# Kernel optimization log

Measured on AMD Instinct MI355X. Metric: run time of the kernel, lower is better.

## Reference

```python
import jax, jax.numpy as jnp
import numpy as np

N, E, D = 50000, 800000, 128
LN_EPS = 1e-5


def setup_inputs() -> dict:
    key = jax.random.key(0)
    ks = jax.random.split(key, 6)
    return {
        "x": jax.random.normal(ks[0], (N, D), dtype=jnp.float32),
        "edge_index": jax.random.randint(ks[1], (2, E), 0, N, dtype=jnp.int64),
        "edge_weight": jax.random.uniform(ks[2], (E,), dtype=jnp.float32),
        "lin_w": jax.random.normal(ks[3], (D, D), dtype=jnp.float32) * (1.0 / np.sqrt(D)),
        "lin_b": jax.random.normal(ks[4], (D,), dtype=jnp.float32) * 0.02,
        "ln_gamma": jnp.ones((D,), dtype=jnp.float32),
        "ln_beta": jnp.zeros((D,), dtype=jnp.float32),
    }


def reference(x, edge_index, edge_weight, lin_w, lin_b, ln_gamma, ln_beta):
    n = x.shape[0]
    src, dst = edge_index[0], edge_index[1]
    # degree (by dst), symmetric-ish normalization with +1 smoothing
    deg = jax.ops.segment_sum(jnp.ones(dst.shape, x.dtype), dst, num_segments=n)
    dis = jax.lax.rsqrt(deg + 1.0)  # (N,)
    # gather -> scale -> scatter-add
    scale = (edge_weight * dis[src])[:, None]          # (E,1)
    msg = x[src] * scale                               # (E,D)
    agg = jax.ops.segment_sum(msg, dst, num_segments=n)  # (N,D)
    agg = agg * dis[:, None] + x                       # residual
    # dense tail: Linear -> GELU (exact, matches torch F.gelu) -> LayerNorm
    h = jax.nn.gelu(agg @ lin_w.T + lin_b, approximate=False)
    mu = jnp.mean(h, axis=-1, keepdims=True)
    var = jnp.mean(jnp.square(h - mu), axis=-1, keepdims=True)
    return (h - mu) * jax.lax.rsqrt(var + LN_EPS) * ln_gamma + ln_beta
```

## Files before the change

### kernel.cpp

```cpp
#include <hip/hip_runtime.h>
#include <hip/hip_fp16.h>
#include <math.h>

#define D 128
#define CAP 48
#define LDS_STRIDE 136
#define CHUNKS 256
#define BLDS 4096

typedef __bf16  bf16x8 __attribute__((ext_vector_type(8)));
typedef float   f32x4  __attribute__((ext_vector_type(4)));

static __device__ __forceinline__ unsigned short f2bf(float f) {
    unsigned int u = __float_as_uint(f);
    u = (u + 0x7fffu + ((u >> 16) & 1u)) >> 16;
    return (unsigned short)u;
}
static __device__ __forceinline__ unsigned int pack2bf(float lo, float hi) {
    return (unsigned int)f2bf(lo) | ((unsigned int)f2bf(hi) << 16);
}
static __device__ __forceinline__ float bflo(unsigned int u) { return __uint_as_float(u << 16); }
static __device__ __forceinline__ float bfhi(unsigned int u) { return __uint_as_float(u & 0xffff0000u); }


__global__ __launch_bounds__(256) void k_hist(const int* __restrict__ dst,
                                              int* __restrict__ H,
                                              int e_count, int cs, int nbk) {
    __shared__ int hist[1024];
    int tid = threadIdx.x, c = blockIdx.x;
    for (int b = tid; b < nbk; b += 256) hist[b] = 0;
    __syncthreads();
    int lo = c * cs, hi = min(lo + cs, e_count);
    for (int i = lo + tid; i < hi; i += 256) atomicAdd(&hist[dst[i] >> 6], 1);
    __syncthreads();
    for (int b = tid; b < nbk; b += 256) H[b * CHUNKS + c] = hist[b];
}

__global__ __launch_bounds__(256) void k_bsum(const int* __restrict__ a,
                                              int* __restrict__ bsum, int n) {
    int g = blockIdx.x * 256 + threadIdx.x;
    int lane = threadIdx.x & 63, wave = threadIdx.x >> 6;
    int v = (g < n) ? a[g] : 0;
    #pragma unroll
    for (int off = 32; off > 0; off >>= 1) v += __shfl_down(v, off);
    __shared__ int ws[4];
    if (lane == 0) ws[wave] = v;
    __syncthreads();
    if (threadIdx.x == 0) bsum[blockIdx.x] = ws[0] + ws[1] + ws[2] + ws[3];
}

__global__ __launch_bounds__(1024) void k_scan_bsum2(int* __restrict__ bsum, int nb) {
    int tid = threadIdx.x, lane = tid & 63, wave = tid >> 6;
    int v = (tid < nb) ? bsum[tid] : 0;
    int incl = v;
    #pragma unroll
    for (int off = 1; off < 64; off <<= 1) {
        int t = __shfl_up(incl, off);
        if (lane >= off) incl += t;
    }
    __shared__ int ws[16];
    if (lane == 63) ws[wave] = incl;
    __syncthreads();
    if (tid == 0) {
        int run = 0;
        #pragma unroll
        for (int i = 0; i < 16; ++i) { int t = ws[i]; ws[i] = run; run += t; }
    }
    __syncthreads();
    if (tid < nb) bsum[tid] = incl - v + ws[wave];
}

__global__ __launch_bounds__(256) void k_applyH(int* __restrict__ H,
                                                const int* __restrict__ bsum_excl, int m) {
    int g = blockIdx.x * 256 + threadIdx.x;
    int tid = threadIdx.x, lane = tid & 63, wave = tid >> 6;
    int v = (g < m) ? H[g] : 0;
    int incl = v;
    #pragma unroll
    for (int off = 1; off < 64; off <<= 1) {
        int t = __shfl_up(incl, off);
        if (lane >= off) incl += t;
    }
    __shared__ int ws[4];
    if (lane == 63) ws[wave] = incl;
    __syncthreads();
    int add = bsum_excl[blockIdx.x];
    for (int i = 0; i < wave; ++i) add += ws[i];
    if (g < m) H[g] = incl - v + add;
}

__global__ __launch_bounds__(256) void k_scatter(const int* __restrict__ src,
                                                 const int* __restrict__ dst,
                                                 const float* __restrict__ ew,
                                                 const int* __restrict__ H,
                                                 unsigned int* __restrict__ rec,
                                                 int e_count, int cs, int nbk) {
    __shared__ int cur[1024];
    int tid = threadIdx.x, c = blockIdx.x;
    for (int b = tid; b < nbk; b += 256) cur[b] = H[b * CHUNKS + c];
    __syncthreads();
    int lo = c * cs, hi = min(lo + cs, e_count);
    for (int i = lo + tid; i < hi; i += 256) {
        int d = dst[i];
        int s = src[i];
        unsigned int q = (unsigned int)(ew[i] * 1023.0f + 0.5f);
        unsigned int r = (q << 22) | ((unsigned int)(d & 63) << 16) | (unsigned int)s;
        int pos = atomicAdd(&cur[d >> 6], 1);
        rec[pos] = r;
    }
}

__global__ __launch_bounds__(256) void k_bucket_sort(unsigned int* __restrict__ rec,
                                                     const int* __restrict__ H,
                                                     int* __restrict__ deg,
                                                     int* __restrict__ offs,
                                                     int e_count, int n, int nbk) {
    __shared__ int hist[64], curs[64];
    __shared__ unsigned int srt[BLDS];
    int tid = threadIdx.x, b = blockIdx.x;
    int start = H[b * CHUNKS];
    int end = (b == nbk - 1) ? e_count : H[(b + 1) * CHUNKS];
    int cnt = min(end - start, BLDS);
    if (tid < 64) hist[tid] = 0;
    __syncthreads();
    for (int i = tid; i < cnt; i += 256) atomicAdd(&hist[(rec[start + i] >> 16) & 63], 1);
    __syncthreads();
    if (tid < 64) {
        int dg = hist[tid];
        int incl = dg;
        #pragma unroll
        for (int off = 1; off < 64; off <<= 1) {
            int t = __shfl_up(incl, off);
            if (tid >= off) incl += t;
        }
        int excl = incl - dg;
        curs[tid] = excl;
        int node = b * 64 + tid;
        if (node < n) {
            deg[node] = dg;
            offs[node] = start + excl;
            if (node == n - 1) offs[n] = e_count;
        }
    }
    __syncthreads();
    for (int i = tid; i < cnt; i += 256) {
        unsigned int r = rec[start + i];
        int rank = atomicAdd(&curs[(r >> 16) & 63], 1);
        srt[rank] = r;
    }
    __syncthreads();
    for (int i = tid; i < cnt; i += 256) rec[start + i] = srt[i];
}


__global__ __launch_bounds__(256) void k_cast(const float* __restrict__ x,
                                              const int* __restrict__ deg,
                                              unsigned short* __restrict__ xs, int n) {
    int i4 = blockIdx.x * 256 + threadIdx.x;
    int nq = n * (D / 4);
    if (i4 >= nq) return;
    int node = i4 >> 5;
    float dd = rsqrtf((float)deg[node] + 1.0f);
    float4 v = ((const float4*)x)[i4];
    ushort4 u;
    u.x = f2bf(v.x * dd); u.y = f2bf(v.y * dd);
    u.z = f2bf(v.z * dd); u.w = f2bf(v.w * dd);
    ((ushort4*)xs)[i4] = u;
}


__global__ __launch_bounds__(256) void k_gather_csr(const unsigned short* __restrict__ xs,
                                                    const float* __restrict__ x,
                                                    const int* __restrict__ offs,
                                                    const unsigned int* __restrict__ rec,
                                                    unsigned short* __restrict__ aggbf, int n) {
    int node = (int)((blockIdx.x * blockDim.x + threadIdx.x) >> 6);
    int lane = threadIdx.x & 63;
    if (node >= n) return;
    int beg = offs[node], end = offs[node + 1];
    const float wq = 1.0f / 1023.0f;
    float ax = 0.f, ay = 0.f;

    int e = beg;
    for (; e + 3 < end; e += 4) {
        unsigned int r0 = rec[e + 0], r1 = rec[e + 1], r2 = rec[e + 2], r3 = rec[e + 3];
        unsigned int u0 = ((const unsigned int*)(xs + (size_t)(r0 & 0xffffu) * D))[lane];
        unsigned int u1 = ((const unsigned int*)(xs + (size_t)(r1 & 0xffffu) * D))[lane];
        unsigned int u2 = ((const unsigned int*)(xs + (size_t)(r2 & 0xffffu) * D))[lane];
        unsigned int u3 = ((const unsigned int*)(xs + (size_t)(r3 & 0xffffu) * D))[lane];
        float w0 = (float)(r0 >> 22) * wq;
        float w1 = (float)(r1 >> 22) * wq;
        float w2 = (float)(r2 >> 22) * wq;
        float w3 = (float)(r3 >> 22) * wq;
        ax += w0 * bflo(u0); ay += w0 * bfhi(u0);
        ax += w1 * bflo(u1); ay += w1 * bfhi(u1);
        ax += w2 * bflo(u2); ay += w2 * bfhi(u2);
        ax += w3 * bflo(u3); ay += w3 * bfhi(u3);
    }
    for (; e < end; ++e) {
        unsigned int r = rec[e];
        unsigned int u = ((const unsigned int*)(xs + (size_t)(r & 0xffffu) * D))[lane];
        float w = (float)(r >> 22) * wq;
        ax += w * bflo(u); ay += w * bfhi(u);
    }

    float dd = rsqrtf((float)(end - beg) + 1.0f);
    float2 xv = ((const float2*)(x + (size_t)node * D))[lane];
    ((unsigned int*)(aggbf + (size_t)node * D))[lane] = pack2bf(ax * dd + xv.x, ay * dd + xv.y);
}


__global__ __launch_bounds__(256) void k_tail_bf(const unsigned short* __restrict__ aggbf,
                                                 float* __restrict__ out,
                                                 const float* __restrict__ W,
                                                 const float* __restrict__ bias,
                                                 const float* __restrict__ gamma,
                                                 const float* __restrict__ beta, int n) {
    __shared__ unsigned short Bl[128 * LDS_STRIDE];

    int tid  = threadIdx.x;
    int lane = tid & 63;
    int wave = tid >> 6;
    int n16  = lane & 15;
    int quad = lane >> 4;

    #pragma unroll
    for (int it = 0; it < 16; ++it) {
        int idx4 = it * 256 + tid;
        float4 w4 = ((const float4*)W)[idx4];
        int t  = idx4 >> 5;
        int k4 = (idx4 & 31) << 2;
        ushort4 u;
        u.x = f2bf(w4.x); u.y = f2bf(w4.y); u.z = f2bf(w4.z); u.w = f2bf(w4.w);
        *(ushort4*)&Bl[t * LDS_STRIDE + k4] = u;
    }
    __syncthreads();

    int row0w = blockIdx.x * 64 + wave * 16;
    int arow  = row0w + n16;

    bf16x8 afr[4];
    #pragma unroll
    for (int ko = 0; ko < 4; ++ko)
        afr[ko] = __builtin_bit_cast(bf16x8,
            *(const uint4*)&aggbf[(size_t)arow * D + ko * 32 + quad * 8]);

    f32x4 acc[8];
    #pragma unroll
    for (int nt = 0; nt < 8; ++nt) acc[nt] = (f32x4){0.f, 0.f, 0.f, 0.f};

    #pragma unroll
    for (int nt = 0; nt < 8; ++nt) {
        #pragma unroll
        for (int ko = 0; ko < 4; ++ko) {
            bf16x8 bfr = __builtin_bit_cast(bf16x8,
                *(const uint4*)&Bl[(nt * 16 + n16) * LDS_STRIDE + ko * 32 + quad * 8]);
            acc[nt] = __builtin_amdgcn_mfma_f32_16x16x32_bf16(afr[ko], bfr, acc[nt], 0, 0, 0);
        }
    }

    float bcol[8], gcol[8], betcol[8];
    #pragma unroll
    for (int nt = 0; nt < 8; ++nt) {
        int col = nt * 16 + n16;
        bcol[nt]   = bias[col];
        gcol[nt]   = gamma[col];
        betcol[nt] = beta[col];
    }

    #pragma unroll
    for (int r = 0; r < 4; ++r) {
        float h[8];
        float s1 = 0.f, s2 = 0.f;
        #pragma unroll
        for (int nt = 0; nt < 8; ++nt) {
            float v = acc[nt][r] + bcol[nt];
            v = 0.5f * v * (1.0f + erff(v * 0.70710678118654752f));
            h[nt] = v;
            s1 += v; s2 += v * v;
        }
        #pragma unroll
        for (int mask = 1; mask < 16; mask <<= 1) {
            s1 += __shfl_xor(s1, mask);
            s2 += __shfl_xor(s2, mask);
        }
        float mu  = s1 * (1.0f / 128.0f);
        float var = s2 * (1.0f / 128.0f) - mu * mu;
        float inv = rsqrtf(var + 1e-5f);
        int row = row0w + quad * 4 + r;
        if (row < n) {
            #pragma unroll
            for (int nt = 0; nt < 8; ++nt)
                out[(size_t)row * D + nt * 16 + n16] = (h[nt] - mu) * inv * gcol[nt] + betcol[nt];
        }
    }
}


__global__ __launch_bounds__(256) void k_fillp8(const int* __restrict__ src,
                                                const int* __restrict__ dst,
                                                const float* __restrict__ ew,
                                                int* __restrict__ cnt,
                                                int2* __restrict__ rec, int e_count) {
    int e = blockIdx.x * blockDim.x + threadIdx.x;
    if (e >= e_count) return;
    int d = dst[e];
    int pos = atomicAdd(&cnt[d], 1);
    if (pos < CAP)
        rec[(size_t)d * CAP + pos] = make_int2(src[e], __float_as_int(ew[e]));
}

__global__ __launch_bounds__(256) void k_gatherp_f32(const float* __restrict__ x,
                                                     const int* __restrict__ cnt,
                                                     const int2* __restrict__ rec,
                                                     float* __restrict__ agg, int n) {
    int node = (int)((blockIdx.x * blockDim.x + threadIdx.x) >> 6);
    int lane = threadIdx.x & 63;
    if (node >= n) return;
    int c = cnt[node];
    int m = min(c, CAP);
    size_t base = (size_t)node * CAP;
    float ax = 0.f, ay = 0.f;
    for (int i = 0; i < m; ++i) {
        int2 p = rec[base + i];
        float w = __int_as_float(p.y) * rsqrtf((float)cnt[p.x] + 1.0f);
        float2 v = ((const float2*)(x + (size_t)p.x * D))[lane];
        ax += w * v.x; ay += w * v.y;
    }
    float dd = rsqrtf((float)c + 1.0f);
    float2 xv = ((const float2*)(x + (size_t)node * D))[lane];
    float2 o;
    o.x = ax * dd + xv.x;
    o.y = ay * dd + xv.y;
    ((float2*)(agg + (size_t)node * D))[lane] = o;
}

__global__ __launch_bounds__(256) void k_tail_mfma(float* __restrict__ io,
                                                   const float* __restrict__ W,
                                                   const float* __restrict__ bias,
                                                   const float* __restrict__ gamma,
                                                   const float* __restrict__ beta, int n) {
    __shared__ unsigned short Bl[128 * LDS_STRIDE];
    __shared__ unsigned short Al[4][16 * LDS_STRIDE];

    int tid  = threadIdx.x;
    int lane = tid & 63;
    int wave = tid >> 6;
    int n16  = lane & 15;
    int quad = lane >> 4;

    #pragma unroll
    for (int it = 0; it < 16; ++it) {
        int idx4 = it * 256 + tid;
        float4 w4 = ((const float4*)W)[idx4];
        int t  = idx4 >> 5;
        int k4 = (idx4 & 31) << 2;
        ushort4 u;
        u.x = f2bf(w4.x); u.y = f2bf(w4.y); u.z = f2bf(w4.z); u.w = f2bf(w4.w);
        *(ushort4*)&Bl[t * LDS_STRIDE + k4] = u;
    }
    int row0w = blockIdx.x * 64 + wave * 16;
    #pragma unroll
    for (int j = 0; j < 8; ++j) {
        int idx4 = j * 64 + lane;
        int m  = idx4 >> 5;
        int k4 = (idx4 & 31) << 2;
        int row = row0w + m;
        float4 a4 = make_float4(0.f, 0.f, 0.f, 0.f);
        if (row < n) a4 = ((const float4*)(io + (size_t)row * D))[idx4 & 31];
        ushort4 u;
        u.x = f2bf(a4.x); u.y = f2bf(a4.y); u.z = f2bf(a4.z); u.w = f2bf(a4.w);
        *(ushort4*)&Al[wave][m * LDS_STRIDE + k4] = u;
    }
    __syncthreads();

    bf16x8 afr[4];
    #pragma unroll
    for (int ko = 0; ko < 4; ++ko)
        afr[ko] = __builtin_bit_cast(bf16x8,
            *(const uint4*)&Al[wave][n16 * LDS_STRIDE + ko * 32 + quad * 8]);

    f32x4 acc[8];
    #pragma unroll
    for (int nt = 0; nt < 8; ++nt) acc[nt] = (f32x4){0.f, 0.f, 0.f, 0.f};

    #pragma unroll
    for (int nt = 0; nt < 8; ++nt) {
        #pragma unroll
        for (int ko = 0; ko < 4; ++ko) {
            bf16x8 bfr = __builtin_bit_cast(bf16x8,
                *(const uint4*)&Bl[(nt * 16 + n16) * LDS_STRIDE + ko * 32 + quad * 8]);
            acc[nt] = __builtin_amdgcn_mfma_f32_16x16x32_bf16(afr[ko], bfr, acc[nt], 0, 0, 0);
        }
    }

    float bcol[8], gcol[8], betcol[8];
    #pragma unroll
    for (int nt = 0; nt < 8; ++nt) {
        int col = nt * 16 + n16;
        bcol[nt]   = bias[col];
        gcol[nt]   = gamma[col];
        betcol[nt] = beta[col];
    }

    #pragma unroll
    for (int r = 0; r < 4; ++r) {
        float h[8];
        float s1 = 0.f, s2 = 0.f;
        #pragma unroll
        for (int nt = 0; nt < 8; ++nt) {
            float v = acc[nt][r] + bcol[nt];
            v = 0.5f * v * (1.0f + erff(v * 0.70710678118654752f));
            h[nt] = v;
            s1 += v; s2 += v * v;
        }
        #pragma unroll
        for (int mask = 1; mask < 16; mask <<= 1) {
            s1 += __shfl_xor(s1, mask);
            s2 += __shfl_xor(s2, mask);
        }
        float mu  = s1 * (1.0f / 128.0f);
        float var = s2 * (1.0f / 128.0f) - mu * mu;
        float inv = rsqrtf(var + 1e-5f);
        int row = row0w + quad * 4 + r;
        if (row < n) {
            #pragma unroll
            for (int nt = 0; nt < 8; ++nt)
                io[(size_t)row * D + nt * 16 + n16] = (h[nt] - mu) * inv * gcol[nt] + betcol[nt];
        }
    }
}


extern "C" void kernel_launch(void* const* d_in, const int* in_sizes, int n_in,
                              void* d_out, int out_size, void* d_ws, size_t ws_size,
                              hipStream_t stream) {
    const float* x    = (const float*)d_in[0];
    const int*   ei   = (const int*)d_in[1];
    const float* ew   = (const float*)d_in[2];
    const float* linw = (const float*)d_in[3];
    const float* linb = (const float*)d_in[4];
    const float* lng  = (const float*)d_in[5];
    const float* lnb  = (const float*)d_in[6];
    float* out = (float*)d_out;

    int n = in_sizes[0] / D;
    int e = in_sizes[1] / 2;
    const int* src = ei;
    const int* dst = ei + e;

    int nbk = (n + 63) / 64;
    int m   = nbk * CHUNKS;
    int cs  = (e + CHUNKS - 1) / CHUNKS;
    int gb  = (n + 3) / 4;
    int tb  = (n + 63) / 64;

    char* wsp = (char*)d_ws;
    size_t off = 0;
    auto alloc = [&](size_t bytes) { char* p = wsp + off; off = (off + bytes + 255) & ~(size_t)255; return p; };
    int*            H     = (int*)alloc((size_t)m * 4);
    int*            bsumH = (int*)alloc((size_t)nbk * 4);
    unsigned int*   rec   = (unsigned int*)alloc((size_t)e * 4);
    int*            deg   = (int*)alloc((size_t)n * 4);
    int*            offs  = (int*)alloc((size_t)(n + 1) * 4);
    unsigned short* xs    = (unsigned short*)alloc((size_t)n * D * 2);
    unsigned short* aggbf = (unsigned short*)alloc(((size_t)n + 64) * D * 2);
    bool big = (off <= ws_size) && (n <= 65535) && (nbk <= 1024);

    if (big) {
        k_hist<<<CHUNKS, 256, 0, stream>>>(dst, H, e, cs, nbk);
        k_bsum<<<nbk, 256, 0, stream>>>(H, bsumH, m);
        k_scan_bsum2<<<1, 1024, 0, stream>>>(bsumH, nbk);
        k_applyH<<<nbk, 256, 0, stream>>>(H, bsumH, m);
        k_scatter<<<CHUNKS, 256, 0, stream>>>(src, dst, ew, H, rec, e, cs, nbk);
        k_bucket_sort<<<nbk, 256, 0, stream>>>(rec, H, deg, offs, e, n, nbk);
        int cb = (n * (D / 4) + 255) / 256;
        k_cast<<<cb, 256, 0, stream>>>(x, deg, xs, n);
        k_gather_csr<<<gb, 256, 0, stream>>>(xs, x, offs, rec, aggbf, n);
        k_tail_bf<<<tb, 256, 0, stream>>>(aggbf, out, linw, linb, lng, lnb, n);
    } else {
        size_t off2 = 0;
        auto alloc2 = [&](size_t bytes) { char* p = wsp + off2; off2 = (off2 + bytes + 255) & ~(size_t)255; return p; };
        int*  cnt2 = (int*)alloc2((size_t)n * 4);
        int2* rec8 = (int2*)alloc2((size_t)n * CAP * 8);
        hipMemsetAsync(cnt2, 0, (size_t)n * 4, stream);
        int eb = (e + 255) / 256;
        k_fillp8<<<eb, 256, 0, stream>>>(src, dst, ew, cnt2, rec8, e);
        k_gatherp_f32<<<gb, 256, 0, stream>>>(x, cnt2, rec8, out, n);
        k_tail_mfma<<<tb, 256, 0, stream>>>(out, linw, linb, lng, lnb, n);
    }
}
```

Before: 175.4 us.

## Fuse bucket sort, CSR gather and dense tail into one per-bucket kernel

Merges the per-bucket local sort, neighbor gather and the MFMA Linear+GELU+LayerNorm tail into one kernel that keeps sorted records and aggregated rows in LDS. This removes the global write-back of sorted records and of the bf16 aggregate. The histogram kernel now also computes degrees and bucket sums with atomics, which drops the separate bsum kernel. The weight matrix is pre-cast to bf16 inside the cast kernel. Each block now gathers 64 nodes with only 4 waves, so gather parallelism is much lower, and the larger LDS footprint may reduce occupancy.

Result: slower. 243.0 us (+38.5%).

```diff
diff --git a/kernel.cpp b/kernel.cpp
--- a/kernel.cpp
+++ b/kernel.cpp
@@ -1,5 +1,4 @@
 #include <hip/hip_runtime.h>
-#include <hip/hip_fp16.h>
 #include <math.h>
 
 #define D 128
@@ -7,6 +6,7 @@
 #define LDS_STRIDE 136
 #define CHUNKS 256
 #define BLDS 4096
+#define ASTR 136
 
 typedef __bf16  bf16x8 __attribute__((ext_vector_type(8)));
 typedef float   f32x4  __attribute__((ext_vector_type(4)));
@@ -23,30 +23,27 @@
 static __device__ __forceinline__ float bfhi(unsigned int u) { return __uint_as_float(u & 0xffff0000u); }
 
 
-__global__ __launch_bounds__(256) void k_hist(const int* __restrict__ dst,
-                                              int* __restrict__ H,
-                                              int e_count, int cs, int nbk) {
+__global__ __launch_bounds__(1024) void k_hist(const int* __restrict__ dst,
+                                               int* __restrict__ H,
+                                               int* __restrict__ deg,
+                                               int* __restrict__ bsum,
+                                               int e_count, int cs, int nbk) {
     __shared__ int hist[1024];
     int tid = threadIdx.x, c = blockIdx.x;
-    for (int b = tid; b < nbk; b += 256) hist[b] = 0;
+    for (int b = tid; b < nbk; b += 1024) hist[b] = 0;
     __syncthreads();
     int lo = c * cs, hi = min(lo + cs, e_count);
-    for (int i = lo + tid; i < hi; i += 256) atomicAdd(&hist[dst[i] >> 6], 1);
-    __syncthreads();
-    for (int b = tid; b < nbk; b += 256) H[b * CHUNKS + c] = hist[b];
-}
-
-__global__ __launch_bounds__(256) void k_bsum(const int* __restrict__ a,
-                                              int* __restrict__ bsum, int n) {
-    int g = blockIdx.x * 256 + threadIdx.x;
-    int lane = threadIdx.x & 63, wave = threadIdx.x >> 6;
-    int v = (g < n) ? a[g] : 0;
-    #pragma unroll
-    for (int off = 32; off > 0; off >>= 1) v += __shfl_down(v, off);
-    __shared__ int ws[4];
-    if (lane == 0) ws[wave] = v;
-    __syncthreads();
-    if (threadIdx.x == 0) bsum[blockIdx.x] = ws[0] + ws[1] + ws[2] + ws[3];
+    for (int i = lo + tid; i < hi; i += 1024) {
+        int d = dst[i];
+        atomicAdd(&hist[d >> 6], 1);
+        atomicAdd(&deg[d], 1);
+    }
+    __syncthreads();
+    for (int b = tid; b < nbk; b += 1024) {
+        int v = hist[b];
+        H[b * CHUNKS + c] = v;
+        if (v) atomicAdd(&bsum[b], v);
+    }
 }
 
 __global__ __launch_bounds__(1024) void k_scan_bsum2(int* __restrict__ bsum, int nb) {
@@ -89,18 +86,18 @@
     if (g < m) H[g] = incl - v + add;
 }
 
-__global__ __launch_bounds__(256) void k_scatter(const int* __restrict__ src,
-                                                 const int* __restrict__ dst,
-                                                 const float* __restrict__ ew,
-                                                 const int* __restrict__ H,
-                                                 unsigned int* __restrict__ rec,
-                                                 int e_count, int cs, int nbk) {
+__global__ __launch_bounds__(1024) void k_scatter(const int* __restrict__ src,
+                                                  const int* __restrict__ dst,
+                                                  const float* __restrict__ ew,
+                                                  const int* __restrict__ H,
+                                                  unsigned int* __restrict__ rec,
+                                                  int e_count, int cs, int nbk) {
     __shared__ int cur[1024];
     int tid = threadIdx.x, c = blockIdx.x;
-    for (int b = tid; b < nbk; b += 256) cur[b] = H[b * CHUNKS + c];
+    for (int b = tid; b < nbk; b += 1024) cur[b] = H[b * CHUNKS + c];
     __syncthreads();
     int lo = c * cs, hi = min(lo + cs, e_count);
-    for (int i = lo + tid; i < hi; i += 256) {
+    for (int i = lo + tid; i < hi; i += 1024) {
         int d = dst[i];
         int s = src[i];
         unsigned int q = (unsigned int)(ew[i] * 1023.0f + 0.5f);
@@ -110,17 +107,59 @@
     }
 }
 
-__global__ __launch_bounds__(256) void k_bucket_sort(unsigned int* __restrict__ rec,
-                                                     const int* __restrict__ H,
-                                                     int* __restrict__ deg,
-                                                     int* __restrict__ offs,
-                                                     int e_count, int n, int nbk) {
-    __shared__ int hist[64], curs[64];
-    __shared__ unsigned int srt[BLDS];
-    int tid = threadIdx.x, b = blockIdx.x;
+
+__global__ __launch_bounds__(256) void k_cast(const float* __restrict__ x,
+                                              const int* __restrict__ deg,
+                                              unsigned short* __restrict__ xs,
+                                              const float* __restrict__ W,
+                                              unsigned short* __restrict__ Wb, int n) {
+    int i4 = blockIdx.x * 256 + threadIdx.x;
+    int nq = n * (D / 4);
+    if (i4 < nq) {
+        int node = i4 >> 5;
+        float dd = rsqrtf((float)deg[node] + 1.0f);
+        float4 v = ((const float4*)x)[i4];
+        ushort4 u;
+        u.x = f2bf(v.x * dd); u.y = f2bf(v.y * dd);
+        u.z = f2bf(v.z * dd); u.w = f2bf(v.w * dd);
+        ((ushort4*)xs)[i4] = u;
+    } else {
+        int j = i4 - nq;
+        if (j < (D * D / 4)) {
+            float4 v = ((const float4*)W)[j];
+            ushort4 u;
+            u.x = f2bf(v.x); u.y = f2bf(v.y);
+            u.z = f2bf(v.z); u.w = f2bf(v.w);
+            ((ushort4*)Wb)[j] = u;
+        }
+    }
+}
+
+
+__global__ __launch_bounds__(256) void k_fused(const unsigned short* __restrict__ xs,
+                                               const float* __restrict__ x,
+                                               const unsigned int* __restrict__ rec,
+                                               const int* __restrict__ H,
+                                               const unsigned short* __restrict__ Wb,
+                                               const float* __restrict__ bias,
+                                               const float* __restrict__ gamma,
+                                               const float* __restrict__ beta,
+                                               float* __restrict__ out,
+                                               int e_count, int n, int nbk) {
+    __shared__ __align__(16) unsigned char smem[52992];
+    unsigned int*   srt = (unsigned int*)smem;
+    unsigned short* Bl  = (unsigned short*)smem;
+    unsigned short* Al  = (unsigned short*)(smem + 34816);
+    int* hist  = (int*)(smem + 52224);
+    int* loffs = (int*)(smem + 52480);
+    int* curs  = (int*)(smem + 52736);
+
+    int tid = threadIdx.x, lane = tid & 63, wave = tid >> 6;
+    int b = blockIdx.x;
     int start = H[b * CHUNKS];
     int end = (b == nbk - 1) ? e_count : H[(b + 1) * CHUNKS];
     int cnt = min(end - start, BLDS);
+
     if (tid < 64) hist[tid] = 0;
     __syncthreads();
     for (int i = tid; i < cnt; i += 256) atomicAdd(&hist[(rec[start + i] >> 16) & 63], 1);
@@ -133,14 +172,8 @@
             int t = __shfl_up(incl, off);
             if (tid >= off) incl += t;
         }
-        int excl = incl - dg;
-        curs[tid] = excl;
-        int node = b * 64 + tid;
-        if (node < n) {
-            deg[node] = dg;
-            offs[node] = start + excl;
-            if (node == n - 1) offs[n] = e_count;
-        }
+        loffs[tid] = incl - dg;
+        curs[tid]  = incl - dg;
     }
     __syncthreads();
     for (int i = tid; i < cnt; i += 256) {
@@ -149,101 +182,66 @@
         srt[rank] = r;
     }
     __syncthreads();
-    for (int i = tid; i < cnt; i += 256) rec[start + i] = srt[i];
-}
-
-
-__global__ __launch_bounds__(256) void k_cast(const float* __restrict__ x,
-                                              const int* __restrict__ deg,
-                                              unsigned short* __restrict__ xs, int n) {
-    int i4 = blockIdx.x * 256 + threadIdx.x;
-    int nq = n * (D / 4);
-    if (i4 >= nq) return;
-    int node = i4 >> 5;
-    float dd = rsqrtf((float)deg[node] + 1.0f);
-    float4 v = ((const float4*)x)[i4];
-    ushort4 u;
-    u.x = f2bf(v.x * dd); u.y = f2bf(v.y * dd);
-    u.z = f2bf(v.z * dd); u.w = f2bf(v.w * dd);
-    ((ushort4*)xs)[i4] = u;
-}
-
-
-__global__ __launch_bounds__(256) void k_gather_csr(const unsigned short* __restrict__ xs,
-                                                    const float* __restrict__ x,
-                                                    const int* __restrict__ offs,
-                                                    const unsigned int* __restrict__ rec,
-                                                    unsigned short* __restrict__ aggbf, int n) {
-    int node = (int)((blockIdx.x * blockDim.x + threadIdx.x) >> 6);
-    int lane = threadIdx.x & 63;
-    if (node >= n) return;
-    int beg = offs[node], end = offs[node + 1];
+
     const float wq = 1.0f / 1023.0f;
-    float ax = 0.f, ay = 0.f;
-
-    int e = beg;
-    for (; e + 3 < end; e += 4) {
-        unsigned int r0 = rec[e + 0], r1 = rec[e + 1], r2 = rec[e + 2], r3 = rec[e + 3];
-        unsigned int u0 = ((const unsigned int*)(xs + (size_t)(r0 & 0xffffu) * D))[lane];
-        unsigned int u1 = ((const unsigned int*)(xs + (size_t)(r1 & 0xffffu) * D))[lane];
-        unsigned int u2 = ((const unsigned int*)(xs + (size_t)(r2 & 0xffffu) * D))[lane];
-        unsigned int u3 = ((const unsigned int*)(xs + (size_t)(r3 & 0xffffu) * D))[lane];
-        float w0 = (float)(r0 >> 22) * wq;
-        float w1 = (float)(r1 >> 22) * wq;
-        float w2 = (float)(r2 >> 22) * wq;
-        float w3 = (float)(r3 >> 22) * wq;
-        ax += w0 * bflo(u0); ay += w0 * bfhi(u0);
-        ax += w1 * bflo(u1); ay += w1 * bfhi(u1);
-        ax += w2 * bflo(u2); ay += w2 * bfhi(u2);
-        ax += w3 * bflo(u3); ay += w3 * bfhi(u3);
-    }
-    for (; e < end; ++e) {
-        unsigned int r = rec[e];
-        unsigned int u = ((const unsigned int*)(xs + (size_t)(r & 0xffffu) * D))[lane];
-        float w = (float)(r >> 22) * wq;
-        ax += w * bflo(u); ay += w * bfhi(u);
-    }
-
-    float dd = rsqrtf((float)(end - beg) + 1.0f);
-    float2 xv = ((const float2*)(x + (size_t)node * D))[lane];
-    ((unsigned int*)(aggbf + (size_t)node * D))[lane] = pack2bf(ax * dd + xv.x, ay * dd + xv.y);
-}
-
-
-__global__ __launch_bounds__(256) void k_tail_bf(const unsigned short* __restrict__ aggbf,
-                                                 float* __restrict__ out,
-                                                 const float* __restrict__ W,
-                                                 const float* __restrict__ bias,
-                                                 const float* __restrict__ gamma,
-                                                 const float* __restrict__ beta, int n) {
-    __shared__ unsigned short Bl[128 * LDS_STRIDE];
-
-    int tid  = threadIdx.x;
-    int lane = tid & 63;
-    int wave = tid >> 6;
-    int n16  = lane & 15;
-    int quad = lane >> 4;
-
-    #pragma unroll
-    for (int it = 0; it < 16; ++it) {
-        int idx4 = it * 256 + tid;
-        float4 w4 = ((const float4*)W)[idx4];
-        int t  = idx4 >> 5;
-        int k4 = (idx4 & 31) << 2;
-        ushort4 u;
-        u.x = f2bf(w4.x); u.y = f2bf(w4.y); u.z = f2bf(w4.z); u.w = f2bf(w4.w);
-        *(ushort4*)&Bl[t * LDS_STRIDE + k4] = u;
-    }
-    __syncthreads();
-
-    int row0w = blockIdx.x * 64 + wave * 16;
-    int arow  = row0w + n16;
+    unsigned short* Aw = Al + wave * (16 * ASTR);
+
+    #pragma unroll 1
+    for (int m = 0; m < 16; ++m) {
+        int lm = wave * 16 + m;
+        int node = b * 64 + lm;
+        unsigned int packed = 0u;
+        if (node < n) {
+            int sbeg = sbeg = loffs[lm];
+            int dcnt = hist[lm];
+            int send = sbeg + dcnt;
+            float ax = 0.f, ay = 0.f;
+            int i = sbeg;
+            for (; i + 7 < send; i += 8) {
+                unsigned int rr[8], uu[8];
+                #pragma unroll
+                for (int j = 0; j < 8; ++j) rr[j] = srt[i + j];
+                #pragma unroll
+                for (int j = 0; j < 8; ++j)
+                    uu[j] = ((const unsigned int*)(xs + (size_t)(rr[j] & 0xffffu) * D))[lane];
+                #pragma unroll
+                for (int j = 0; j < 8; ++j) {
+                    float w = (float)(rr[j] >> 22) * wq;
+                    ax += w * bflo(uu[j]); ay += w * bfhi(uu[j]);
+                }
+            }
+            for (; i < send; ++i) {
+                unsigned int r = srt[i];
+                unsigned int u = ((const unsigned int*)(xs + (size_t)(r & 0xffffu) * D))[lane];
+                float w = (float)(r >> 22) * wq;
+                ax += w * bflo(u); ay += w * bfhi(u);
+            }
+            float dd = rsqrtf((float)dcnt + 1.0f);
+            float2 xv = ((const float2*)(x + (size_t)node * D))[lane];
+            packed = pack2bf(ax * dd + xv.x, ay * dd + xv.y);
+        }
+        ((unsigned int*)(Aw + m * ASTR))[lane] = packed;
+    }
+
+    __syncthreads();
+
+    #pragma unroll
+    for (int it = 0; it < 8; ++it) {
+        int idx = it * 256 + tid;
+        uint4 w4 = ((const uint4*)Wb)[idx];
+        int t  = idx >> 4;
+        int k8 = (idx & 15) << 3;
+        *(uint4*)&Bl[t * ASTR + k8] = w4;
+    }
+    __syncthreads();
+
+    int n16 = lane & 15, quad = lane >> 4;
 
     bf16x8 afr[4];
     #pragma unroll
     for (int ko = 0; ko < 4; ++ko)
         afr[ko] = __builtin_bit_cast(bf16x8,
-            *(const uint4*)&aggbf[(size_t)arow * D + ko * 32 + quad * 8]);
+            *(const uint4*)&Aw[n16 * ASTR + ko * 32 + quad * 8]);
 
     f32x4 acc[8];
     #pragma unroll
@@ -254,7 +252,7 @@
         #pragma unroll
         for (int ko = 0; ko < 4; ++ko) {
             bf16x8 bfr = __builtin_bit_cast(bf16x8,
-                *(const uint4*)&Bl[(nt * 16 + n16) * LDS_STRIDE + ko * 32 + quad * 8]);
+                *(const uint4*)&Bl[(nt * 16 + n16) * ASTR + ko * 32 + quad * 8]);
             acc[nt] = __builtin_amdgcn_mfma_f32_16x16x32_bf16(afr[ko], bfr, acc[nt], 0, 0, 0);
         }
     }
@@ -268,6 +266,7 @@
         betcol[nt] = beta[col];
     }
 
+    int row0w = b * 64 + wave * 16;
     #pragma unroll
     for (int r = 0; r < 4; ++r) {
         float h[8];
@@ -452,32 +451,28 @@
     int nbk = (n + 63) / 64;
     int m   = nbk * CHUNKS;
     int cs  = (e + CHUNKS - 1) / CHUNKS;
-    int gb  = (n + 3) / 4;
-    int tb  = (n + 63) / 64;
 
     char* wsp = (char*)d_ws;
     size_t off = 0;
     auto alloc = [&](size_t bytes) { char* p = wsp + off; off = (off + bytes + 255) & ~(size_t)255; return p; };
     int*            H     = (int*)alloc((size_t)m * 4);
     int*            bsumH = (int*)alloc((size_t)nbk * 4);
+    int*            deg   = (int*)alloc((size_t)n * 4);
     unsigned int*   rec   = (unsigned int*)alloc((size_t)e * 4);
-    int*            deg   = (int*)alloc((size_t)n * 4);
-    int*            offs  = (int*)alloc((size_t)(n + 1) * 4);
     unsigned short* xs    = (unsigned short*)alloc((size_t)n * D * 2);
-    unsigned short* aggbf = (unsigned short*)alloc(((size_t)n + 64) * D * 2);
+    unsigned short* Wb    = (unsigned short*)alloc((size_t)D * D * 2);
     bool big = (off <= ws_size) && (n <= 65535) && (nbk <= 1024);
 
     if (big) {
-        k_hist<<<CHUNKS, 256, 0, stream>>>(dst, H, e, cs, nbk);
-        k_bsum<<<nbk, 256, 0, stream>>>(H, bsumH, m);
+        size_t zspan = (size_t)((char*)deg - (char*)bsumH) + (size_t)n * 4;
+        hipMemsetAsync(bsumH, 0, zspan, stream);
+        k_hist<<<CHUNKS, 1024, 0, stream>>>(dst, H, deg, bsumH, e, cs, nbk);
         k_scan_bsum2<<<1, 1024, 0, stream>>>(bsumH, nbk);
         k_applyH<<<nbk, 256, 0, stream>>>(H, bsumH, m);
-        k_scatter<<<CHUNKS, 256, 0, stream>>>(src, dst, ew, H, rec, e, cs, nbk);
-        k_bucket_sort<<<nbk, 256, 0, stream>>>(rec, H, deg, offs, e, n, nbk);
-        int cb = (n * (D / 4) + 255) / 256;
-        k_cast<<<cb, 256, 0, stream>>>(x, deg, xs, n);
-        k_gather_csr<<<gb, 256, 0, stream>>>(xs, x, offs, rec, aggbf, n);
-        k_tail_bf<<<tb, 256, 0, stream>>>(aggbf, out, linw, linb, lng, lnb, n);
+        int cb = (n * (D / 4) + (D * D / 4) + 255) / 256;
+        k_cast<<<cb, 256, 0, stream>>>(x, deg, xs, linw, Wb, n);
+        k_scatter<<<CHUNKS, 1024, 0, stream>>>(src, dst, ew, H, rec, e, cs, nbk);
+        k_fused<<<nbk, 256, 0, stream>>>(xs, x, rec, H, Wb, linb, lng, lnb, out, e, n, nbk);
     } else {
         size_t off2 = 0;
         auto alloc2 = [&](size_t bytes) { char* p = wsp + off2; off2 = (off2 + bytes + 255) & ~(size_t)255; return p; };
@@ -485,6 +480,8 @@
         int2* rec8 = (int2*)alloc2((size_t)n * CAP * 8);
         hipMemsetAsync(cnt2, 0, (size_t)n * 4, stream);
         int eb = (e + 255) / 256;
+        int gb = (n + 3) / 4;
+        int tb = (n + 63) / 64;
         k_fillp8<<<eb, 256, 0, stream>>>(src, dst, ew, cnt2, rec8, e);
         k_gatherp_f32<<<gb, 256, 0, stream>>>(x, cnt2, rec8, out, n);
         k_tail_mfma<<<tb, 256, 0, stream>>>(out, linw, linb, lng, lnb, n);
```

## Fuse bucket-sum into histogram, pre-cast weights once, enlarge blocks to 1024 threads

Applied to the files above, without the earlier changes.

The k_bsum kernel is dropped. k_hist now adds each nonzero per-chunk bucket count atomically into bsum, after a memset clears it. The linear weight is converted to bf16 once inside k_cast instead of in every k_tail_bf block, which now copies pre-cast bf16 rows into LDS. Histogram, scatter and tail kernels move to 1024-thread blocks, with the tail covering 256 rows per block. This removes one launch and the repeated per-block weight conversion, at the cost of global atomics on bsum and fewer, larger blocks that may reduce occupancy and latency hiding.

Result: slower. 181.4 us (+3.4%).

```diff
diff --git a/kernel.cpp b/kernel.cpp
--- a/kernel.cpp
+++ b/kernel.cpp
@@ -1,5 +1,4 @@
 #include <hip/hip_runtime.h>
-#include <hip/hip_fp16.h>
 #include <math.h>
 
 #define D 128
@@ -23,30 +22,22 @@
 static __device__ __forceinline__ float bfhi(unsigned int u) { return __uint_as_float(u & 0xffff0000u); }
 
 
-__global__ __launch_bounds__(256) void k_hist(const int* __restrict__ dst,
-                                              int* __restrict__ H,
-                                              int e_count, int cs, int nbk) {
+__global__ __launch_bounds__(1024) void k_hist(const int* __restrict__ dst,
+                                               int* __restrict__ H,
+                                               int* __restrict__ bsum,
+                                               int e_count, int cs, int nbk) {
     __shared__ int hist[1024];
     int tid = threadIdx.x, c = blockIdx.x;
-    for (int b = tid; b < nbk; b += 256) hist[b] = 0;
+    for (int b = tid; b < nbk; b += 1024) hist[b] = 0;
     __syncthreads();
     int lo = c * cs, hi = min(lo + cs, e_count);
-    for (int i = lo + tid; i < hi; i += 256) atomicAdd(&hist[dst[i] >> 6], 1);
-    __syncthreads();
-    for (int b = tid; b < nbk; b += 256) H[b * CHUNKS + c] = hist[b];
-}
-
-__global__ __launch_bounds__(256) void k_bsum(const int* __restrict__ a,
-                                              int* __restrict__ bsum, int n) {
-    int g = blockIdx.x * 256 + threadIdx.x;
-    int lane = threadIdx.x & 63, wave = threadIdx.x >> 6;
-    int v = (g < n) ? a[g] : 0;
-    #pragma unroll
-    for (int off = 32; off > 0; off >>= 1) v += __shfl_down(v, off);
-    __shared__ int ws[4];
-    if (lane == 0) ws[wave] = v;
-    __syncthreads();
-    if (threadIdx.x == 0) bsum[blockIdx.x] = ws[0] + ws[1] + ws[2] + ws[3];
+    for (int i = lo + tid; i < hi; i += 1024) atomicAdd(&hist[dst[i] >> 6], 1);
+    __syncthreads();
+    for (int b = tid; b < nbk; b += 1024) {
+        int v = hist[b];
+        H[b * CHUNKS + c] = v;
+        if (v) atomicAdd(&bsum[b], v);
+    }
 }
 
 __global__ __launch_bounds__(1024) void k_scan_bsum2(int* __restrict__ bsum, int nb) {
@@ -89,18 +80,18 @@
     if (g < m) H[g] = incl - v + add;
 }
 
-__global__ __launch_bounds__(256) void k_scatter(const int* __restrict__ src,
-                                                 const int* __restrict__ dst,
-                                                 const float* __restrict__ ew,
-                                                 const int* __restrict__ H,
-                                                 unsigned int* __restrict__ rec,
-                                                 int e_count, int cs, int nbk) {
+__global__ __launch_bounds__(1024) void k_scatter(const int* __restrict__ src,
+                                                  const int* __restrict__ dst,
+                                                  const float* __restrict__ ew,
+                                                  const int* __restrict__ H,
+                                                  unsigned int* __restrict__ rec,
+                                                  int e_count, int cs, int nbk) {
     __shared__ int cur[1024];
     int tid = threadIdx.x, c = blockIdx.x;
-    for (int b = tid; b < nbk; b += 256) cur[b] = H[b * CHUNKS + c];
+    for (int b = tid; b < nbk; b += 1024) cur[b] = H[b * CHUNKS + c];
     __syncthreads();
     int lo = c * cs, hi = min(lo + cs, e_count);
-    for (int i = lo + tid; i < hi; i += 256) {
+    for (int i = lo + tid; i < hi; i += 1024) {
         int d = dst[i];
         int s = src[i];
         unsigned int q = (unsigned int)(ew[i] * 1023.0f + 0.5f);
@@ -155,17 +146,29 @@
 
 __global__ __launch_bounds__(256) void k_cast(const float* __restrict__ x,
                                               const int* __restrict__ deg,
-                                              unsigned short* __restrict__ xs, int n) {
+                                              unsigned short* __restrict__ xs,
+                                              const float* __restrict__ W,
+                                              unsigned short* __restrict__ Wb, int n) {
     int i4 = blockIdx.x * 256 + threadIdx.x;
     int nq = n * (D / 4);
-    if (i4 >= nq) return;
-    int node = i4 >> 5;
-    float dd = rsqrtf((float)deg[node] + 1.0f);
-    float4 v = ((const float4*)x)[i4];
-    ushort4 u;
-    u.x = f2bf(v.x * dd); u.y = f2bf(v.y * dd);
-    u.z = f2bf(v.z * dd); u.w = f2bf(v.w * dd);
-    ((ushort4*)xs)[i4] = u;
+    if (i4 < nq) {
+        int node = i4 >> 5;
+        float dd = rsqrtf((float)deg[node] + 1.0f);
+        float4 v = ((const float4*)x)[i4];
+        ushort4 u;
+        u.x = f2bf(v.x * dd); u.y = f2bf(v.y * dd);
+        u.z = f2bf(v.z * dd); u.w = f2bf(v.w * dd);
+        ((ushort4*)xs)[i4] = u;
+    } else {
+        int j = i4 - nq;
+        if (j < (D * D / 4)) {
+            float4 v = ((const float4*)W)[j];
+            ushort4 u;
+            u.x = f2bf(v.x); u.y = f2bf(v.y);
+            u.z = f2bf(v.z); u.w = f2bf(v.w);
+            ((ushort4*)Wb)[j] = u;
+        }
+    }
 }
 
 
@@ -210,12 +213,12 @@
 }
 
 
-__global__ __launch_bounds__(256) void k_tail_bf(const unsigned short* __restrict__ aggbf,
-                                                 float* __restrict__ out,
-                                                 const float* __restrict__ W,
-                                                 const float* __restrict__ bias,
-                                                 const float* __restrict__ gamma,
-                                                 const float* __restrict__ beta, int n) {
+__global__ __launch_bounds__(1024) void k_tail_bf(const unsigned short* __restrict__ aggbf,
+                                                  float* __restrict__ out,
+                                                  const unsigned short* __restrict__ Wb,
+                                                  const float* __restrict__ bias,
+                                                  const float* __restrict__ gamma,
+                                                  const float* __restrict__ beta, int n) {
     __shared__ unsigned short Bl[128 * LDS_STRIDE];
 
     int tid  = threadIdx.x;
@@ -225,18 +228,16 @@
     int quad = lane >> 4;
 
     #pragma unroll
-    for (int it = 0; it < 16; ++it) {
-        int idx4 = it * 256 + tid;
-        float4 w4 = ((const float4*)W)[idx4];
-        int t  = idx4 >> 5;
-        int k4 = (idx4 & 31) << 2;
-        ushort4 u;
-        u.x = f2bf(w4.x); u.y = f2bf(w4.y); u.z = f2bf(w4.z); u.w = f2bf(w4.w);
-        *(ushort4*)&Bl[t * LDS_STRIDE + k4] = u;
-    }
-    __syncthreads();
-
-    int row0w = blockIdx.x * 64 + wave * 16;
+    for (int it = 0; it < 2; ++it) {
+        int idx = it * 1024 + tid;
+        uint4 w4 = ((const uint4*)Wb)[idx];
+        int t  = idx >> 4;
+        int k8 = (idx & 15) << 3;
+        *(uint4*)&Bl[t * LDS_STRIDE + k8] = w4;
+    }
+    __syncthreads();
+
+    int row0w = blockIdx.x * 256 + wave * 16;
     int arow  = row0w + n16;
 
     bf16x8 afr[4];
@@ -453,7 +454,7 @@
     int m   = nbk * CHUNKS;
     int cs  = (e + CHUNKS - 1) / CHUNKS;
     int gb  = (n + 3) / 4;
-    int tb  = (n + 63) / 64;
+    int tb  = (n + 255) / 256;
 
     char* wsp = (char*)d_ws;
     size_t off = 0;
@@ -464,20 +465,21 @@
     int*            deg   = (int*)alloc((size_t)n * 4);
     int*            offs  = (int*)alloc((size_t)(n + 1) * 4);
     unsigned short* xs    = (unsigned short*)alloc((size_t)n * D * 2);
-    unsigned short* aggbf = (unsigned short*)alloc(((size_t)n + 64) * D * 2);
+    unsigned short* Wb    = (unsigned short*)alloc((size_t)D * D * 2);
+    unsigned short* aggbf = (unsigned short*)alloc(((size_t)n + 256) * D * 2);
     bool big = (off <= ws_size) && (n <= 65535) && (nbk <= 1024);
 
     if (big) {
-        k_hist<<<CHUNKS, 256, 0, stream>>>(dst, H, e, cs, nbk);
-        k_bsum<<<nbk, 256, 0, stream>>>(H, bsumH, m);
+        hipMemsetAsync(bsumH, 0, (size_t)nbk * 4, stream);
+        k_hist<<<CHUNKS, 1024, 0, stream>>>(dst, H, bsumH, e, cs, nbk);
         k_scan_bsum2<<<1, 1024, 0, stream>>>(bsumH, nbk);
         k_applyH<<<nbk, 256, 0, stream>>>(H, bsumH, m);
-        k_scatter<<<CHUNKS, 256, 0, stream>>>(src, dst, ew, H, rec, e, cs, nbk);
+        k_scatter<<<CHUNKS, 1024, 0, stream>>>(src, dst, ew, H, rec, e, cs, nbk);
         k_bucket_sort<<<nbk, 256, 0, stream>>>(rec, H, deg, offs, e, n, nbk);
-        int cb = (n * (D / 4) + 255) / 256;
-        k_cast<<<cb, 256, 0, stream>>>(x, deg, xs, n);
+        int cb = (n * (D / 4) + (D * D / 4) + 255) / 256;
+        k_cast<<<cb, 256, 0, stream>>>(x, deg, xs, linw, Wb, n);
         k_gather_csr<<<gb, 256, 0, stream>>>(xs, x, offs, rec, aggbf, n);
-        k_tail_bf<<<tb, 256, 0, stream>>>(aggbf, out, linw, linb, lng, lnb, n);
+        k_tail_bf<<<tb, 1024, 0, stream>>>(aggbf, out, Wb, linb, lng, lnb, n);
     } else {
         size_t off2 = 0;
         auto alloc2 = [&](size_t bytes) { char* p = wsp + off2; off2 = (off2 + bytes + 255) & ~(size_t)255; return p; };
@@ -485,8 +487,9 @@
         int2* rec8 = (int2*)alloc2((size_t)n * CAP * 8);
         hipMemsetAsync(cnt2, 0, (size_t)n * 4, stream);
         int eb = (e + 255) / 256;
+        int tb64 = (n + 63) / 64;
         k_fillp8<<<eb, 256, 0, stream>>>(src, dst, ew, cnt2, rec8, e);
         k_gatherp_f32<<<gb, 256, 0, stream>>>(x, cnt2, rec8, out, n);
-        k_tail_mfma<<<tb, 256, 0, stream>>>(out, linw, linb, lng, lnb, n);
-    }
-}
+        k_tail_mfma<<<tb64, 256, 0, stream>>>(out, linw, linb, lng, lnb, n);
+    }
+}
```
